# Kernel tuning notes

Measured on AMD Instinct MI355X. Metric: run time of the kernel, lower is better.

The kernel has to match this reference:

```python
import jax, jax.numpy as jnp
import numpy as np

N = 50000
E = 800000
IN_DIM = 128
OUT_DIM = 128
HEADS = 4
HEAD_DIM = OUT_DIM // HEADS  # 32


def setup_inputs() -> dict:
    key = jax.random.key(0)
    k1, k2, k3, k4 = jax.random.split(key, 4)
    x = jax.random.normal(k1, (N, IN_DIM), dtype=jnp.float32)
    edge_index = jax.random.randint(k2, (2, E), 0, N, dtype=jnp.int32)
    # nn.Linear(in_dim, out_dim): weight [out_dim, in_dim]
    W = jax.random.normal(k3, (OUT_DIM, IN_DIM), dtype=jnp.float32) * (1.0 / np.sqrt(IN_DIM))
    # nn.Linear(2*head_dim, 1): weight [1, 2*head_dim] -> flattened [2*head_dim]
    a_w = jax.random.normal(k4, (2 * HEAD_DIM,), dtype=jnp.float32) * (1.0 / np.sqrt(2 * HEAD_DIM))
    return {"x": x, "edge_index": edge_index, "W": W, "a_w": a_w}


def reference(x, edge_index, W, a_w):
    n = x.shape[0]
    Wx = (x @ W.T).reshape(n, HEADS, HEAD_DIM)          # [N,H,D]
    src, dst = edge_index[0], edge_index[1]
    Wx_src = Wx[src]                                     # [E,H,D]
    Wx_dst = Wx[dst]                                     # [E,H,D]
    # a([Wx_src || Wx_dst]) = Wx_src @ a_src + Wx_dst @ a_dst
    a_src, a_dst = a_w[:HEAD_DIM], a_w[HEAD_DIM:]
    e = jnp.einsum('ehd,d->eh', Wx_src, a_src) + jnp.einsum('ehd,d->eh', Wx_dst, a_dst)
    e = jax.nn.leaky_relu(e, negative_slope=0.2)         # [E,H]
    # numerically-stable segment softmax over incoming edges of each dst node
    e_max = jax.ops.segment_max(e, dst, num_segments=n)  # [N,H], -inf for empty
    e_exp = jnp.exp(e - e_max[dst])                      # [E,H]
    denom = jax.ops.segment_sum(e_exp, dst, num_segments=n)  # [N,H]
    alpha = e_exp / (denom[dst] + 1e-8)                  # [E,H] (dropout=0 -> identity)
    weighted = alpha[..., None] * Wx_src                 # [E,H,D]
    out = jax.ops.segment_sum(weighted, dst, num_segments=n)  # [N,H,D]
    return jax.nn.elu(out.reshape(n, OUT_DIM))
```

## Files before the change

### kernel.cpp

```cpp
#include <hip/hip_runtime.h>
#include <hip/hip_bf16.h>
#include <math.h>

#define HEADS 4
#define NBKT 196
#define CAPB 4608
#define CAPP 6656

typedef short bf16x8 __attribute__((ext_vector_type(8)));
typedef float f32x4 __attribute__((ext_vector_type(4)));
typedef unsigned short ushort8 __attribute__((ext_vector_type(8)));

__device__ __forceinline__ float lrelu(float v) { return v >= 0.f ? v : 0.2f * v; }

__device__ __forceinline__ unsigned short f2bf(float f) {
    unsigned u = __float_as_uint(f);
    return (unsigned short)((u + 0x7FFF + ((u >> 16) & 1)) >> 16);
}

__device__ __forceinline__ unsigned pk2bf(float a, float b) {
    __hip_bfloat162 h = __float22bfloat162_rn(make_float2(a, b));
    unsigned u;
    __builtin_memcpy(&u, &h, 4);
    return u;
}

__global__ __launch_bounds__(256, 2) void fused_kernel(const float* __restrict__ x,
                                                       const float* __restrict__ W,
                                                       const float* __restrict__ aw,
                                                       const int* __restrict__ ei,
                                                       unsigned short* __restrict__ Wxh,
                                                       float* __restrict__ s_src,
                                                       float* __restrict__ s_dst,
                                                       int* __restrict__ gcur,
                                                       unsigned* __restrict__ gbuf,
                                                       int n, int E, int ngemm) {
    __shared__ __align__(16) char smem[66304];
    const int t = threadIdx.x;

    if ((int)blockIdx.x < ngemm) {
        unsigned short* Alds = (unsigned short*)smem;
        unsigned short* Blds = (unsigned short*)(smem + 32768);
        float* sawm = (float*)(smem + 65536);
        const int w = t >> 6, l = t & 63;
        const int q = l >> 4, l16 = l & 15;
        const int node0 = blockIdx.x * 128;

        if (t < 64) sawm[t] = aw[t];

#pragma unroll
        for (int i = 0; i < 8; ++i) {
            int c = i * 256 + t;
            int nl = c >> 4, k8 = c & 15;
            int gn = node0 + nl;
            if (gn >= n) gn = n - 1;
            const float4* gp = (const float4*)(x + (size_t)gn * 128 + k8 * 8);
            float4 v0 = gp[0], v1 = gp[1];
            uint4 u = make_uint4(pk2bf(v0.x, v0.y), pk2bf(v0.z, v0.w),
                                 pk2bf(v1.x, v1.y), pk2bf(v1.z, v1.w));
            int ch = (((nl >> 4) * 4 + (k8 >> 2)) * 4 + (k8 & 3)) * 16 + (nl & 15);
            *(uint4*)(&Alds[ch * 8]) = u;
        }
#pragma unroll
        for (int i = 0; i < 8; ++i) {
            int c = i * 256 + t;
            int dl = c >> 4, k8 = c & 15;
            const float4* gp = (const float4*)(W + (size_t)dl * 128 + k8 * 8);
            float4 v0 = gp[0], v1 = gp[1];
            uint4 u = make_uint4(pk2bf(v0.x, v0.y), pk2bf(v0.z, v0.w),
                                 pk2bf(v1.x, v1.y), pk2bf(v1.z, v1.w));
            int ch = (((dl >> 4) * 4 + (k8 >> 2)) * 4 + (k8 & 3)) * 16 + (dl & 15);
            *(uint4*)(&Blds[ch * 8]) = u;
        }
        __syncthreads();

        f32x4 acc[2][8];
#pragma unroll
        for (int rt = 0; rt < 2; ++rt)
#pragma unroll
            for (int ct = 0; ct < 8; ++ct) acc[rt][ct] = (f32x4){0.f, 0.f, 0.f, 0.f};

#pragma unroll
        for (int kk = 0; kk < 4; ++kk) {
            bf16x8 a0 = *(const bf16x8*)(&Alds[(((w * 2 + 0) * 4 + kk) * 64 + l) * 8]);
            bf16x8 a1 = *(const bf16x8*)(&Alds[(((w * 2 + 1) * 4 + kk) * 64 + l) * 8]);
#pragma unroll
            for (int ct = 0; ct < 8; ++ct) {
                bf16x8 b = *(const bf16x8*)(&Blds[((ct * 4 + kk) * 64 + l) * 8]);
                acc[0][ct] = __builtin_amdgcn_mfma_f32_16x16x32_bf16(a0, b, acc[0][ct], 0, 0, 0);
                acc[1][ct] = __builtin_amdgcn_mfma_f32_16x16x32_bf16(a1, b, acc[1][ct], 0, 0, 0);
            }
        }

        __syncthreads();
#pragma unroll
        for (int rt = 0; rt < 2; ++rt) {
            int nl = w * 32 + rt * 16 + q * 4;
#pragma unroll
            for (int ct = 0; ct < 8; ++ct) {
                int dim = ct * 16 + l16;
                Alds[(nl + 0) * 128 + dim] = f2bf(acc[rt][ct][0]);
                Alds[(nl + 1) * 128 + dim] = f2bf(acc[rt][ct][1]);
                Alds[(nl + 2) * 128 + dim] = f2bf(acc[rt][ct][2]);
                Alds[(nl + 3) * 128 + dim] = f2bf(acc[rt][ct][3]);
            }
        }
        __syncthreads();

#pragma unroll
        for (int i = 0; i < 8; ++i) {
            int c = i * 256 + t;
            int nl = c >> 4, d8 = c & 15;
            int gn = node0 + nl;
            ushort8 u = *(const ushort8*)(&Alds[nl * 128 + d8 * 8]);
            if (gn < n) *(ushort8*)(Wxh + (size_t)gn * 128 + d8 * 8) = u;
            float sp = 0.f, dp = 0.f;
            int ab = (d8 & 3) * 8;
#pragma unroll
            for (int j = 0; j < 8; ++j) {
                float v = __uint_as_float(((unsigned)(unsigned short)u[j]) << 16);
                sp += v * sawm[ab + j];
                dp += v * sawm[32 + ab + j];
            }
            sp += __shfl_xor(sp, 1, 64); dp += __shfl_xor(dp, 1, 64);
            sp += __shfl_xor(sp, 2, 64); dp += __shfl_xor(dp, 2, 64);
            if ((l & 3) == 0 && gn < n) {
                int h = (l & 15) >> 2;
                s_src[(size_t)gn * 4 + h] = sp;
                s_dst[(size_t)gn * 4 + h] = dp;
            }
        }
    } else {
        int* hist = (int*)smem;
        int* scanws = (int*)(smem + 1024);
        int* lbase = (int*)(smem + 2048);
        int* lcur = (int*)(smem + 3072);
        int* gb = (int*)(smem + 4096);
        unsigned* sorted = (unsigned*)(smem + 5120);
        unsigned char* bkt = (unsigned char*)(smem + 21504);

        const int blk = blockIdx.x - ngemm;
        const int b0 = blk * 4096;
        const int total = min(4096, E - b0);

        hist[t] = 0;
        __syncthreads();

        unsigned pk[16];
#pragma unroll
        for (int i = 0; i < 16; ++i) {
            int idx = i * 256 + t;
            if (idx < total) {
                int e = b0 + idx;
                unsigned s = (unsigned)ei[e], d = (unsigned)ei[E + e];
                pk[i] = s | (d << 16);
                atomicAdd(&hist[d >> 8], 1);
            }
        }
        __syncthreads();
        int v = hist[t];
        scanws[t] = v;
        __syncthreads();
        for (int off = 1; off < 256; off <<= 1) {
            int y = (t >= off) ? scanws[t - off] : 0;
            __syncthreads();
            scanws[t] += y;
            __syncthreads();
        }
        int ex = scanws[t] - v;
        lbase[t] = ex;
        lcur[t] = ex;
        if (t < NBKT) gb[t] = (v > 0) ? atomicAdd(&gcur[t], v) : 0;
        __syncthreads();
#pragma unroll
        for (int i = 0; i < 16; ++i) {
            int idx = i * 256 + t;
            if (idx < total) {
                int b = pk[i] >> 24;
                int qpos = atomicAdd(&lcur[b], 1);
                sorted[qpos] = pk[i];
                bkt[qpos] = (unsigned char)b;
            }
        }
        __syncthreads();
#pragma unroll
        for (int i = 0; i < 16; ++i) {
            int s = i * 256 + t;
            if (s < total) {
                int b = bkt[s];
                int pos = gb[b] + (s - lbase[b]);
                if (pos < CAPB) gbuf[(size_t)b * CAPB + pos] = sorted[s];
            }
        }
    }
}

__global__ __launch_bounds__(1024) void pass2_kernel(const int* __restrict__ gcur,
                                                     const unsigned* __restrict__ gbuf,
                                                     unsigned short* __restrict__ csr,
                                                     int2* __restrict__ node_info,
                                                     float* __restrict__ s_src, int n) {
    __shared__ int hist[256], scanws[256], cur[256];
    const int t = threadIdx.x;
    const int bucket = blockIdx.x;
    int cnt = gcur[bucket];
    if (cnt > CAPB) cnt = CAPB;
    const unsigned* gp = gbuf + (size_t)bucket * CAPB;

    if (bucket == 0 && t < 4) s_src[(size_t)n * 4 + t] = -1e30f;

    if (t < 256) hist[t] = 0;
    __syncthreads();

    unsigned e[5];
#pragma unroll
    for (int i = 0; i < 5; ++i) {
        int idx = i * 1024 + t;
        if (idx < cnt) {
            e[i] = gp[idx];
            atomicAdd(&hist[(e[i] >> 16) & 255], 1);
        }
    }
    __syncthreads();
    int v = 0, vp = 0;
    if (t < 256) {
        v = hist[t];
        vp = (v + 7) & ~7;
        scanws[t] = vp;
    }
    __syncthreads();
    for (int off = 1; off < 256; off <<= 1) {
        int y = 0;
        if (t < 256 && t >= off) y = scanws[t - off];
        __syncthreads();
        if (t < 256) scanws[t] += y;
        __syncthreads();
    }
    if (t < 256) {
        int ex = scanws[t] - vp;
        cur[t] = ex;
        int node = bucket * 256 + t;
        if (node < n) node_info[node] = make_int2(bucket * CAPP + ex, vp);
        for (int j = v; j < vp; ++j) csr[(size_t)bucket * CAPP + ex + j] = (unsigned short)n;
    }
    __syncthreads();
#pragma unroll
    for (int i = 0; i < 5; ++i) {
        int idx = i * 1024 + t;
        if (idx < cnt) {
            int ld = (e[i] >> 16) & 255;
            int qpos = atomicAdd(&cur[ld], 1);
            csr[(size_t)bucket * CAPP + qpos] = (unsigned short)(e[i] & 0xFFFF);
        }
    }
}

__global__ __launch_bounds__(256) void accum_kernel(const int2* __restrict__ node_info,
                                                    const unsigned short* __restrict__ csr,
                                                    const float* __restrict__ s_src,
                                                    const float* __restrict__ s_dst,
                                                    const unsigned short* __restrict__ Wxh,
                                                    float* __restrict__ out, int n) {
    int wid = threadIdx.x >> 6, lane = threadIdx.x & 63;
    int node = blockIdx.x * 4 + wid;
    if (node >= n) return;
    int l = lane & 15, grp = lane >> 4;
    int h = l >> 2;
    int2 info = node_info[node];
    int start = info.x, npairs = info.y >> 1;
    float sdn = s_dst[(size_t)node * 4 + h];
    const unsigned ONE2 = 0x3F803F80u;

    float acc[8] = {0.f, 0.f, 0.f, 0.f, 0.f, 0.f, 0.f, 0.f};
    float dsum = 0.f;
    int p = grp;
    for (; p + 4 < npairs; p += 8) {
        unsigned c0 = *(const unsigned*)(csr + start + 2 * p);
        unsigned c1 = *(const unsigned*)(csr + start + 2 * (p + 4));
        int sa0 = c0 & 0xFFFF, sa1 = c0 >> 16;
        int sb0 = c1 & 0xFFFF, sb1 = c1 >> 16;
        uint4 Ua0 = *(const uint4*)(Wxh + ((size_t)sa0 << 7) + l * 8);
        uint4 Ua1 = *(const uint4*)(Wxh + ((size_t)sa1 << 7) + l * 8);
        uint4 Ub0 = *(const uint4*)(Wxh + ((size_t)sb0 << 7) + l * 8);
        uint4 Ub1 = *(const uint4*)(Wxh + ((size_t)sb1 << 7) + l * 8);
        float wa0 = __expf(lrelu(s_src[sa0 * 4 + h] + sdn));
        float wa1 = __expf(lrelu(s_src[sa1 * 4 + h] + sdn));
        float wb0 = __expf(lrelu(s_src[sb0 * 4 + h] + sdn));
        float wb1 = __expf(lrelu(s_src[sb1 * 4 + h] + sdn));
        unsigned wpa = pk2bf(wa0, wa1);
        unsigned wpb = pk2bf(wb0, wb1);
        asm("v_dot2_f32_bf16 %0, %1, %2, %0" : "+v"(dsum) : "v"(wpa), "v"(ONE2));
        asm("v_dot2_f32_bf16 %0, %1, %2, %0" : "+v"(dsum) : "v"(wpb), "v"(ONE2));
        unsigned a0[4] = {Ua0.x, Ua0.y, Ua0.z, Ua0.w};
        unsigned a1[4] = {Ua1.x, Ua1.y, Ua1.z, Ua1.w};
        unsigned b0[4] = {Ub0.x, Ub0.y, Ub0.z, Ub0.w};
        unsigned b1[4] = {Ub1.x, Ub1.y, Ub1.z, Ub1.w};
#pragma unroll
        for (int j = 0; j < 4; ++j) {
            unsigned lo_a = __builtin_amdgcn_perm(a0[j], a1[j], 0x01000504u);
            unsigned hi_a = __builtin_amdgcn_perm(a0[j], a1[j], 0x03020706u);
            unsigned lo_b = __builtin_amdgcn_perm(b0[j], b1[j], 0x01000504u);
            unsigned hi_b = __builtin_amdgcn_perm(b0[j], b1[j], 0x03020706u);
            asm("v_dot2_f32_bf16 %0, %1, %2, %0" : "+v"(acc[2 * j]) : "v"(wpa), "v"(lo_a));
            asm("v_dot2_f32_bf16 %0, %1, %2, %0" : "+v"(acc[2 * j + 1]) : "v"(wpa), "v"(hi_a));
            asm("v_dot2_f32_bf16 %0, %1, %2, %0" : "+v"(acc[2 * j]) : "v"(wpb), "v"(lo_b));
            asm("v_dot2_f32_bf16 %0, %1, %2, %0" : "+v"(acc[2 * j + 1]) : "v"(wpb), "v"(hi_b));
        }
    }
    if (p < npairs) {
        unsigned c0 = *(const unsigned*)(csr + start + 2 * p);
        int sa0 = c0 & 0xFFFF, sa1 = c0 >> 16;
        uint4 Ua0 = *(const uint4*)(Wxh + ((size_t)sa0 << 7) + l * 8);
        uint4 Ua1 = *(const uint4*)(Wxh + ((size_t)sa1 << 7) + l * 8);
        float wa0 = __expf(lrelu(s_src[sa0 * 4 + h] + sdn));
        float wa1 = __expf(lrelu(s_src[sa1 * 4 + h] + sdn));
        unsigned wpa = pk2bf(wa0, wa1);
        asm("v_dot2_f32_bf16 %0, %1, %2, %0" : "+v"(dsum) : "v"(wpa), "v"(ONE2));
        unsigned a0[4] = {Ua0.x, Ua0.y, Ua0.z, Ua0.w};
        unsigned a1[4] = {Ua1.x, Ua1.y, Ua1.z, Ua1.w};
#pragma unroll
        for (int j = 0; j < 4; ++j) {
            unsigned lo_a = __builtin_amdgcn_perm(a0[j], a1[j], 0x01000504u);
            unsigned hi_a = __builtin_amdgcn_perm(a0[j], a1[j], 0x03020706u);
            asm("v_dot2_f32_bf16 %0, %1, %2, %0" : "+v"(acc[2 * j]) : "v"(wpa), "v"(lo_a));
            asm("v_dot2_f32_bf16 %0, %1, %2, %0" : "+v"(acc[2 * j + 1]) : "v"(wpa), "v"(hi_a));
        }
    }
#pragma unroll
    for (int m = 16; m <= 32; m <<= 1) {
#pragma unroll
        for (int j = 0; j < 8; ++j) acc[j] += __shfl_xor(acc[j], m, 64);
        dsum += __shfl_xor(dsum, m, 64);
    }
    if (grp == 0) {
        float inv = 1.f / (dsum + 1e-8f);
        float o[8];
#pragma unroll
        for (int j = 0; j < 8; ++j) {
            float v = acc[j] * inv;
            o[j] = v > 0.f ? v : (__expf(v) - 1.f);
        }
        float4* dp = (float4*)(out + (size_t)node * 128 + l * 8);
        dp[0] = make_float4(o[0], o[1], o[2], o[3]);
        dp[1] = make_float4(o[4], o[5], o[6], o[7]);
    }
}

extern "C" void kernel_launch(void* const* d_in, const int* in_sizes, int n_in,
                              void* d_out, int out_size, void* d_ws, size_t ws_size,
                              hipStream_t stream) {
    const float* x = (const float*)d_in[0];
    const int* ei = (const int*)d_in[1];
    const float* W = (const float*)d_in[2];
    const float* aw = (const float*)d_in[3];
    float* out = (float*)d_out;
    const int n = in_sizes[0] / 128;
    const int E = in_sizes[1] / 2;

    char* ws = (char*)d_ws;
    size_t off = 0;
    unsigned short* Wxh = (unsigned short*)(ws + off); off += (size_t)(n + 8) * 128 * 2;
    float* s_src = (float*)(ws + off);     off += (size_t)(n + 1) * HEADS * 4;
    float* s_dst = (float*)(ws + off);     off += (size_t)n * HEADS * 4;
    int* gcur = (int*)(ws + off);          off += 1024;
    unsigned* gbuf = (unsigned*)(ws + off); off += (size_t)NBKT * CAPB * 4;
    unsigned short* csr = (unsigned short*)(ws + off); off += (size_t)NBKT * CAPP * 2;
    int2* node_info = (int2*)(ws + off);   off += (size_t)n * 8;

    const int ngemm = (n + 127) / 128;
    const int npass1 = (E + 4095) / 4096;

    hipMemsetAsync(gcur, 0, 1024, stream);
    fused_kernel<<<ngemm + npass1, 256, 0, stream>>>(x, W, aw, ei, Wxh, s_src, s_dst,
                                                     gcur, gbuf, n, E, ngemm);
    pass2_kernel<<<npass1, 1024, 0, stream>>>(gcur, gbuf, csr, node_info, s_src, n);
    accum_kernel<<<(n + 3) / 4, 256, 0, stream>>>(node_info, csr, s_src, s_dst, Wxh, out, n);
}
```

Baseline: 137.9 us.

## Precompute per-edge attention weights in CSR build pass instead of accumulate kernel

The pass that builds the CSR now also computes the exponentiated leaky-relu attention weights for every edge pair and all four heads. It stores them as packed bf16 in a new buffer laid out parallel to the CSR. The accumulate kernel then reads one dword per pair per head instead of gathering s_src/s_dst and computing exp, which removes the random s_src gathers and redundant exp work from the latency-bound gather loop. In exchange it adds a global write and read of the weight buffer and extra LDS use in pass2. Padding entries now get a weight of zero, so the s_src sentinel write is dropped.

```diff
diff --git a/kernel.cpp b/kernel.cpp
--- a/kernel.cpp
+++ b/kernel.cpp
@@ -197,17 +197,19 @@
 
 __global__ __launch_bounds__(1024) void pass2_kernel(const int* __restrict__ gcur,
                                                      const unsigned* __restrict__ gbuf,
+                                                     const float* __restrict__ s_src,
+                                                     const float* __restrict__ s_dst,
                                                      unsigned short* __restrict__ csr,
-                                                     int2* __restrict__ node_info,
-                                                     float* __restrict__ s_src, int n) {
+                                                     uint4* __restrict__ wbuf4,
+                                                     int2* __restrict__ node_info, int n) {
     __shared__ int hist[256], scanws[256], cur[256];
+    __shared__ unsigned short srcbuf[CAPP];
+    __shared__ unsigned char nodebuf[CAPP];
     const int t = threadIdx.x;
     const int bucket = blockIdx.x;
     int cnt = gcur[bucket];
     if (cnt > CAPB) cnt = CAPB;
     const unsigned* gp = gbuf + (size_t)bucket * CAPB;
-
-    if (bucket == 0 && t < 4) s_src[(size_t)n * 4 + t] = -1e30f;
 
     if (t < 256) hist[t] = 0;
     __syncthreads();
@@ -241,7 +243,11 @@
         cur[t] = ex;
         int node = bucket * 256 + t;
         if (node < n) node_info[node] = make_int2(bucket * CAPP + ex, vp);
-        for (int j = v; j < vp; ++j) csr[(size_t)bucket * CAPP + ex + j] = (unsigned short)n;
+        for (int j = v; j < vp; ++j) {
+            csr[(size_t)bucket * CAPP + ex + j] = (unsigned short)n;
+            srcbuf[ex + j] = (unsigned short)n;
+            nodebuf[ex + j] = (unsigned char)t;
+        }
     }
     __syncthreads();
 #pragma unroll
@@ -250,15 +256,40 @@
         if (idx < cnt) {
             int ld = (e[i] >> 16) & 255;
             int qpos = atomicAdd(&cur[ld], 1);
-            csr[(size_t)bucket * CAPP + qpos] = (unsigned short)(e[i] & 0xFFFF);
-        }
+            unsigned short sv = (unsigned short)(e[i] & 0xFFFF);
+            csr[(size_t)bucket * CAPP + qpos] = sv;
+            srcbuf[qpos] = sv;
+            nodebuf[qpos] = (unsigned char)ld;
+        }
+    }
+    __syncthreads();
+    int totpairs = scanws[255] >> 1;
+    const float4* ss4 = (const float4*)s_src;
+    const float4* sd4 = (const float4*)s_dst;
+    for (int p = t; p < totpairs; p += 1024) {
+        int i0 = 2 * p;
+        int src0 = srcbuf[i0], src1 = srcbuf[i0 + 1];
+        int node = bucket * 256 + nodebuf[i0];
+        float4 sd = sd4[node];
+        bool r0 = src0 < n, r1 = src1 < n;
+        float4 a0 = ss4[r0 ? src0 : 0];
+        float4 a1 = ss4[r1 ? src1 : 0];
+        float w00 = r0 ? __expf(lrelu(a0.x + sd.x)) : 0.f;
+        float w01 = r0 ? __expf(lrelu(a0.y + sd.y)) : 0.f;
+        float w02 = r0 ? __expf(lrelu(a0.z + sd.z)) : 0.f;
+        float w03 = r0 ? __expf(lrelu(a0.w + sd.w)) : 0.f;
+        float w10 = r1 ? __expf(lrelu(a1.x + sd.x)) : 0.f;
+        float w11 = r1 ? __expf(lrelu(a1.y + sd.y)) : 0.f;
+        float w12 = r1 ? __expf(lrelu(a1.z + sd.z)) : 0.f;
+        float w13 = r1 ? __expf(lrelu(a1.w + sd.w)) : 0.f;
+        wbuf4[(size_t)bucket * (CAPP / 2) + p] =
+            make_uint4(pk2bf(w00, w10), pk2bf(w01, w11), pk2bf(w02, w12), pk2bf(w03, w13));
     }
 }
 
 __global__ __launch_bounds__(256) void accum_kernel(const int2* __restrict__ node_info,
                                                     const unsigned short* __restrict__ csr,
-                                                    const float* __restrict__ s_src,
-                                                    const float* __restrict__ s_dst,
+                                                    const unsigned* __restrict__ wdw,
                                                     const unsigned short* __restrict__ Wxh,
                                                     float* __restrict__ out, int n) {
     int wid = threadIdx.x >> 6, lane = threadIdx.x & 63;
@@ -268,7 +299,7 @@
     int h = l >> 2;
     int2 info = node_info[node];
     int start = info.x, npairs = info.y >> 1;
-    float sdn = s_dst[(size_t)node * 4 + h];
+    int s2 = start >> 1;
     const unsigned ONE2 = 0x3F803F80u;
 
     float acc[8] = {0.f, 0.f, 0.f, 0.f, 0.f, 0.f, 0.f, 0.f};
@@ -277,18 +308,14 @@
     for (; p + 4 < npairs; p += 8) {
         unsigned c0 = *(const unsigned*)(csr + start + 2 * p);
         unsigned c1 = *(const unsigned*)(csr + start + 2 * (p + 4));
+        unsigned wpa = wdw[(size_t)(s2 + p) * 4 + h];
+        unsigned wpb = wdw[(size_t)(s2 + p + 4) * 4 + h];
         int sa0 = c0 & 0xFFFF, sa1 = c0 >> 16;
         int sb0 = c1 & 0xFFFF, sb1 = c1 >> 16;
         uint4 Ua0 = *(const uint4*)(Wxh + ((size_t)sa0 << 7) + l * 8);
         uint4 Ua1 = *(const uint4*)(Wxh + ((size_t)sa1 << 7) + l * 8);
         uint4 Ub0 = *(const uint4*)(Wxh + ((size_t)sb0 << 7) + l * 8);
         uint4 Ub1 = *(const uint4*)(Wxh + ((size_t)sb1 << 7) + l * 8);
-        float wa0 = __expf(lrelu(s_src[sa0 * 4 + h] + sdn));
-        float wa1 = __expf(lrelu(s_src[sa1 * 4 + h] + sdn));
-        float wb0 = __expf(lrelu(s_src[sb0 * 4 + h] + sdn));
-        float wb1 = __expf(lrelu(s_src[sb1 * 4 + h] + sdn));
-        unsigned wpa = pk2bf(wa0, wa1);
-        unsigned wpb = pk2bf(wb0, wb1);
         asm("v_dot2_f32_bf16 %0, %1, %2, %0" : "+v"(dsum) : "v"(wpa), "v"(ONE2));
         asm("v_dot2_f32_bf16 %0, %1, %2, %0" : "+v"(dsum) : "v"(wpb), "v"(ONE2));
         unsigned a0[4] = {Ua0.x, Ua0.y, Ua0.z, Ua0.w};
@@ -309,12 +336,10 @@
     }
     if (p < npairs) {
         unsigned c0 = *(const unsigned*)(csr + start + 2 * p);
+        unsigned wpa = wdw[(size_t)(s2 + p) * 4 + h];
         int sa0 = c0 & 0xFFFF, sa1 = c0 >> 16;
         uint4 Ua0 = *(const uint4*)(Wxh + ((size_t)sa0 << 7) + l * 8);
         uint4 Ua1 = *(const uint4*)(Wxh + ((size_t)sa1 << 7) + l * 8);
-        float wa0 = __expf(lrelu(s_src[sa0 * 4 + h] + sdn));
-        float wa1 = __expf(lrelu(s_src[sa1 * 4 + h] + sdn));
-        unsigned wpa = pk2bf(wa0, wa1);
         asm("v_dot2_f32_bf16 %0, %1, %2, %0" : "+v"(dsum) : "v"(wpa), "v"(ONE2));
         unsigned a0[4] = {Ua0.x, Ua0.y, Ua0.z, Ua0.w};
         unsigned a1[4] = {Ua1.x, Ua1.y, Ua1.z, Ua1.w};
@@ -365,6 +390,7 @@
     int* gcur = (int*)(ws + off);          off += 1024;
     unsigned* gbuf = (unsigned*)(ws + off); off += (size_t)NBKT * CAPB * 4;
     unsigned short* csr = (unsigned short*)(ws + off); off += (size_t)NBKT * CAPP * 2;
+    uint4* wbuf4 = (uint4*)(ws + off);     off += (size_t)NBKT * (CAPP / 2) * 16;
     int2* node_info = (int2*)(ws + off);   off += (size_t)n * 8;
 
     const int ngemm = (n + 127) / 128;
@@ -373,6 +399,8 @@
     hipMemsetAsync(gcur, 0, 1024, stream);
     fused_kernel<<<ngemm + npass1, 256, 0, stream>>>(x, W, aw, ei, Wxh, s_src, s_dst,
                                                      gcur, gbuf, n, E, ngemm);
-    pass2_kernel<<<npass1, 1024, 0, stream>>>(gcur, gbuf, csr, node_info, s_src, n);
-    accum_kernel<<<(n + 3) / 4, 256, 0, stream>>>(node_info, csr, s_src, s_dst, Wxh, out, n);
-}
+    pass2_kernel<<<npass1, 1024, 0, stream>>>(gcur, gbuf, s_src, s_dst, csr, wbuf4,
+                                              node_info, n);
+    accum_kernel<<<(n + 3) / 4, 256, 0, stream>>>(node_info, csr, (const unsigned*)wbuf4,
+                                                  Wxh, out, n);
+}
```

New measurement: 142.1 us. 1.03x slower.
